# Kernel tuning notes

Measured on AMD Instinct MI355X. Metric: run time of the kernel, lower is better.

## Reference

```python
import jax, jax.numpy as jnp
import numpy as np

NUM_BITS = 8
NUM_STEPS = 2 ** NUM_BITS - 2  # 254, clamp range -127..127


def _roundpass(x):
    # straight-through round: forward=round, backward=identity
    return x + jax.lax.stop_gradient(jnp.round(x) - x)


def _quantize(x, alpha, always_pos=False):
    # Quantizer.quantize with use_ste=True, is_on=True
    alpha = jax.nn.relu(alpha)  # relu(alpha_baseline + alpha_delta)
    stepsize = 2.0 * alpha / NUM_STEPS
    off = alpha if always_pos else 0.0
    scaled = (x - off) / stepsize
    clamped = jnp.clip(_roundpass(scaled), -(NUM_STEPS // 2), NUM_STEPS // 2)
    return clamped * stepsize + off


def setup_inputs() -> dict:
    key = jax.random.key(0)
    k1, k2 = jax.random.split(key)
    x = jax.random.normal(k1, (32, 64, 56, 56), dtype=jnp.float32)
    w = jax.random.normal(k2, (128, 64, 3, 3), dtype=jnp.float32) * 0.05
    alpha_x = jnp.ones((1,), dtype=jnp.float32)
    alpha_w = jnp.ones((1,), dtype=jnp.float32)
    return {"x": x, "w": w, "alpha_x": alpha_x, "alpha_w": alpha_w}


def reference(x, w, alpha_x, alpha_w):
    # quantize activations and weights (8-bit symmetric, STE round)
    qx = _quantize(x, alpha_x[0], always_pos=False)
    qw = _quantize(w, alpha_w[0], always_pos=False)
    # im2col lowering + tiled_mm accumulation over K-tiles is exactly a
    # stride-1 conv with padding (1,1); tile padding in M/N/K contributes
    # only zeros and is sliced off, so plain conv is the faithful math.
    out = jax.lax.conv_general_dilated(
        qx, qw,
        window_strides=(1, 1),
        padding=((1, 1), (1, 1)),
        dimension_numbers=("NCHW", "OIHW", "NCHW"),
    )  # [32, 128, 56, 56]
    return out
```

## Files before the change

kernel.cpp:

```cpp
#include <hip/hip_runtime.h>
#include <hip/hip_bf16.h>

typedef int   v4i __attribute__((ext_vector_type(4)));
typedef float v4f __attribute__((ext_vector_type(4)));

#define HWSZ 3136
#define IMW  56
#define PADW 58
#define PHW  3364
#define CIN  64
#define COUT 128

__device__ __forceinline__ float step_size(float a) {
    a = a > 0.f ? a : 0.f;
    return 2.0f * a / 254.0f;
}

__device__ __forceinline__ int quant1(float x, float s) {
    float v = rintf(x / s);
    v = fminf(127.f, fmaxf(-127.f, v));
    return (int)v;
}

__device__ __forceinline__ unsigned int pack4(int a, int b, int c, int d) {
    return (unsigned int)(a & 255) | ((unsigned int)(b & 255) << 8) |
           ((unsigned int)(c & 255) << 16) | ((unsigned int)(d & 255) << 24);
}

__device__ __forceinline__ void gload_lds16(const signed char* g, signed char* l) {
    __builtin_amdgcn_global_load_lds(
        (const __attribute__((address_space(1))) void*)g,
        (__attribute__((address_space(3))) void*)l, 16, 0, 0);
}

__global__ __launch_bounds__(256) void quant_kernel(const float* __restrict__ x,
                                                    const float* __restrict__ w,
                                                    const float* __restrict__ alpha_x,
                                                    const float* __restrict__ alpha_w,
                                                    signed char* __restrict__ cx,
                                                    signed char* __restrict__ wt) {
    int t = threadIdx.x;
    int b = blockIdx.x;
    if (b >= 1568) {
        if (b >= 1856) {
            int q = (b - 1856) * 256 + t;
            int n = q / 912;
            int r = q % 912;
            int px = r >> 2, seg = r & 3;
            int ph, pw;
            if (px < 58)       { ph = 0;  pw = px; }
            else if (px < 116) { ph = 57; pw = px - 58; }
            else { int k = px - 116; ph = 1 + (k >> 1); pw = (k & 1) * 57; }
            v4i z = {0, 0, 0, 0};
            *(v4i*)(cx + ((size_t)n * PHW + ph * PADW + pw) * 64 + seg * 16) = z;
            return;
        }
        float s = step_size(alpha_w[0]);
        int j = (b - 1568) * 256 + t;
        int tap = j / 8192;
        int r   = j % 8192;
        int o   = r >> 6;
        int c   = r & 63;
        float v = w[((size_t)o * 64 + c) * 9 + tap];
        wt[j] = (signed char)quant1(v, s);
        return;
    }

    __shared__ unsigned int tile32[64 * 17];
    float s = step_size(alpha_x[0]);
    int n   = b / 49;
    int hw0 = (b % 49) * 64;
    int g   = t & 15;
    int cq  = t >> 4;
    int p   = t >> 2;
    int seg = t & 3;

    const float* xb = x + ((size_t)n * CIN + cq * 4) * HWSZ + hw0 + g * 4;
    v4f f0 = *(const v4f*)(xb);
    v4f f1 = *(const v4f*)(xb + HWSZ);
    v4f f2 = *(const v4f*)(xb + 2 * HWSZ);
    v4f f3 = *(const v4f*)(xb + 3 * HWSZ);
#pragma unroll
    for (int j = 0; j < 4; ++j) {
        unsigned int u = pack4(quant1(f0[j], s), quant1(f1[j], s),
                               quant1(f2[j], s), quant1(f3[j], s));
        tile32[(g * 4 + j) * 17 + cq] = u;
    }
    __syncthreads();
    int base = p * 17 + seg * 4;
    v4i val;
    val[0] = (int)tile32[base + 0];
    val[1] = (int)tile32[base + 1];
    val[2] = (int)tile32[base + 2];
    val[3] = (int)tile32[base + 3];
    int hw = hw0 + p;
    int h = hw / IMW, wq = hw % IMW;
    *(v4i*)(cx + ((size_t)n * PHW + (h + 1) * PADW + (wq + 1)) * 64 + seg * 16) = val;
}

__global__ __launch_bounds__(256, 4) void conv_kernel(const signed char* __restrict__ cx,
                                                      const signed char* __restrict__ wt,
                                                      const float* __restrict__ ax,
                                                      const float* __restrict__ aw,
                                                      float* __restrict__ out) {
    __shared__ __attribute__((aligned(16))) signed char as_[34816];
    float scale = step_size(ax[0]) * step_size(aw[0]);
    int tid  = threadIdx.x;
    int lane = tid & 63;
    int wid  = tid >> 6;
    int row  = lane & 15;
    int kg   = lane >> 4;

    int bid  = blockIdx.x;
    int swz  = (bid & 7) * 196 + (bid >> 3);
    int p0   = swz * 64;
    int n    = p0 / HWSZ;
    int hw0  = p0 % HWSZ;
    int h0   = hw0 / IMW;
    int us   = h0 - 1; if (us > 52) us = 52;

    const signed char* wsrc = cx + ((size_t)n * PHW + (size_t)(us + 1) * PADW) * 64;
#pragma unroll
    for (int r = 0; r < 5; ++r) {
        int slotbase = r * 256 + wid * 64;
        gload_lds16(wsrc + (size_t)(slotbase + lane) * 16, as_ + slotbase * 16);
    }

    int obase = wid * 32;
    const signed char* wb = wt + (obase + row) * 64 + kg * 16;
    v4i breg[9][2];
#pragma unroll
    for (int tap = 0; tap < 9; ++tap)
#pragma unroll
        for (int ot = 0; ot < 2; ++ot)
            breg[tap][ot] = *(const v4i*)(wb + tap * (COUT * 64) + ot * (16 * 64));

    int lbase[4];
#pragma unroll
    for (int pt = 0; pt < 4; ++pt) {
        int hwp = hw0 + pt * 16 + row;
        int hh  = hwp / IMW, ww = hwp % IMW;
        lbase[pt] = ((hh - us) * PADW + (ww + 1)) * 64 + kg * 16;
    }

    asm volatile("s_waitcnt vmcnt(0)" ::: "memory");
    __syncthreads();
#pragma unroll
    for (int tap = 0; tap < 9; ++tap)
#pragma unroll
        for (int ot = 0; ot < 2; ++ot)
            asm volatile("" :: "v"(breg[tap][ot]));

    v4i acc[4][2] = {};
#pragma unroll
    for (int tap = 0; tap < 9; ++tap) {
        int doff = ((tap / 3 - 1) * PADW + (tap % 3 - 1)) * 64;
        v4i a[4];
#pragma unroll
        for (int pt = 0; pt < 4; ++pt)
            a[pt] = *(const v4i*)(as_ + lbase[pt] + doff);
#pragma unroll
        for (int pt = 0; pt < 4; ++pt)
#pragma unroll
            for (int ot = 0; ot < 2; ++ot)
                acc[pt][ot] = __builtin_amdgcn_mfma_i32_16x16x64_i8(a[pt], breg[tap][ot], acc[pt][ot], 0, 0, 0);
    }

    __syncthreads();
    signed char* scrw = as_ + wid * 8704;
    float* obb = out + ((size_t)n * COUT) * HWSZ + hw0;

#pragma unroll
    for (int otl = 0; otl < 2; ++otl) {
        int ol = otl * 16 + row;
#pragma unroll
        for (int pt = 0; pt < 4; ++pt) {
            int c  = pt * 4 + kg;
            int cs = c ^ (ol & 7);
            v4f v;
            v[0] = scale * (float)acc[pt][otl][0];
            v[1] = scale * (float)acc[pt][otl][1];
            v[2] = scale * (float)acc[pt][otl][2];
            v[3] = scale * (float)acc[pt][otl][3];
            *(v4f*)(scrw + ol * 272 + cs * 16) = v;
        }
    }
    {
        int og = lane >> 4;
        int c  = lane & 15;
#pragma unroll
        for (int j = 0; j < 8; ++j) {
            int ol = j * 4 + og;
            int cs = c ^ (ol & 7);
            v4f v = *(const v4f*)(scrw + ol * 272 + cs * 16);
            int o = obase + ol;
            *(v4f*)(obb + (size_t)o * HWSZ + c * 4) = v;
        }
    }
}

extern "C" void kernel_launch(void* const* d_in, const int* in_sizes, int n_in,
                              void* d_out, int out_size, void* d_ws, size_t ws_size,
                              hipStream_t stream) {
    const float* x  = (const float*)d_in[0];
    const float* w  = (const float*)d_in[1];
    const float* ax = (const float*)d_in[2];
    const float* aw = (const float*)d_in[3];
    float* out = (float*)d_out;

    signed char* cx = (signed char*)d_ws;
    signed char* wt = cx + 6889472;

    quant_kernel<<<1970, 256, 0, stream>>>(x, w, ax, aw, cx, wt);
    conv_kernel<<<1568, 256, 0, stream>>>(cx, wt, ax, aw, out);
}
```

Baseline: 29.15 us.

## Fuse activation quantization into conv kernel, drop padded int8 intermediate

Activation quantization and padding move into the conv kernel. Each block loads its five input rows of fp32 straight from x, quantizes them to int8, and writes them transposed into LDS, with zeroed halo rows and columns. This removes the global write and re-read of the padded int8 activation tensor and the extra launch work for it, leaving only a small weight-quantization kernel. In exchange each input row is read and quantized by several overlapping blocks (5 rows loaded per 64-pixel tile, about 4x redundancy in fp32 reads), and the LDS stores are scattered 4-byte writes.

Result: slower. 39.58 us (+35.8%).

```diff
diff --git a/kernel.cpp b/kernel.cpp
--- a/kernel.cpp
+++ b/kernel.cpp
@@ -6,10 +6,9 @@
 
 #define HWSZ 3136
 #define IMW  56
-#define PADW 58
-#define PHW  3364
 #define CIN  64
 #define COUT 128
+#define ROWB 3712
 
 __device__ __forceinline__ float step_size(float a) {
     a = a > 0.f ? a : 0.f;
@@ -27,84 +26,26 @@
            ((unsigned int)(c & 255) << 16) | ((unsigned int)(d & 255) << 24);
 }
 
-__device__ __forceinline__ void gload_lds16(const signed char* g, signed char* l) {
-    __builtin_amdgcn_global_load_lds(
-        (const __attribute__((address_space(1))) void*)g,
-        (__attribute__((address_space(3))) void*)l, 16, 0, 0);
+__global__ __launch_bounds__(256) void quantw_kernel(const float* __restrict__ w,
+                                                     const float* __restrict__ alpha_w,
+                                                     signed char* __restrict__ wt) {
+    float s = step_size(alpha_w[0]);
+    int j = blockIdx.x * 256 + threadIdx.x;
+    int tap = j / 8192;
+    int r   = j % 8192;
+    int o   = r >> 6;
+    int c   = r & 63;
+    wt[j] = (signed char)quant1(w[((size_t)o * 64 + c) * 9 + tap], s);
 }
 
-__global__ __launch_bounds__(256) void quant_kernel(const float* __restrict__ x,
-                                                    const float* __restrict__ w,
-                                                    const float* __restrict__ alpha_x,
-                                                    const float* __restrict__ alpha_w,
-                                                    signed char* __restrict__ cx,
-                                                    signed char* __restrict__ wt) {
-    int t = threadIdx.x;
-    int b = blockIdx.x;
-    if (b >= 1568) {
-        if (b >= 1856) {
-            int q = (b - 1856) * 256 + t;
-            int n = q / 912;
-            int r = q % 912;
-            int px = r >> 2, seg = r & 3;
-            int ph, pw;
-            if (px < 58)       { ph = 0;  pw = px; }
-            else if (px < 116) { ph = 57; pw = px - 58; }
-            else { int k = px - 116; ph = 1 + (k >> 1); pw = (k & 1) * 57; }
-            v4i z = {0, 0, 0, 0};
-            *(v4i*)(cx + ((size_t)n * PHW + ph * PADW + pw) * 64 + seg * 16) = z;
-            return;
-        }
-        float s = step_size(alpha_w[0]);
-        int j = (b - 1568) * 256 + t;
-        int tap = j / 8192;
-        int r   = j % 8192;
-        int o   = r >> 6;
-        int c   = r & 63;
-        float v = w[((size_t)o * 64 + c) * 9 + tap];
-        wt[j] = (signed char)quant1(v, s);
-        return;
-    }
-
-    __shared__ unsigned int tile32[64 * 17];
-    float s = step_size(alpha_x[0]);
-    int n   = b / 49;
-    int hw0 = (b % 49) * 64;
-    int g   = t & 15;
-    int cq  = t >> 4;
-    int p   = t >> 2;
-    int seg = t & 3;
-
-    const float* xb = x + ((size_t)n * CIN + cq * 4) * HWSZ + hw0 + g * 4;
-    v4f f0 = *(const v4f*)(xb);
-    v4f f1 = *(const v4f*)(xb + HWSZ);
-    v4f f2 = *(const v4f*)(xb + 2 * HWSZ);
-    v4f f3 = *(const v4f*)(xb + 3 * HWSZ);
-#pragma unroll
-    for (int j = 0; j < 4; ++j) {
-        unsigned int u = pack4(quant1(f0[j], s), quant1(f1[j], s),
-                               quant1(f2[j], s), quant1(f3[j], s));
-        tile32[(g * 4 + j) * 17 + cq] = u;
-    }
-    __syncthreads();
-    int base = p * 17 + seg * 4;
-    v4i val;
-    val[0] = (int)tile32[base + 0];
-    val[1] = (int)tile32[base + 1];
-    val[2] = (int)tile32[base + 2];
-    val[3] = (int)tile32[base + 3];
-    int hw = hw0 + p;
-    int h = hw / IMW, wq = hw % IMW;
-    *(v4i*)(cx + ((size_t)n * PHW + (h + 1) * PADW + (wq + 1)) * 64 + seg * 16) = val;
-}
-
-__global__ __launch_bounds__(256, 4) void conv_kernel(const signed char* __restrict__ cx,
+__global__ __launch_bounds__(256, 4) void conv_kernel(const float* __restrict__ x,
                                                       const signed char* __restrict__ wt,
                                                       const float* __restrict__ ax,
                                                       const float* __restrict__ aw,
                                                       float* __restrict__ out) {
     __shared__ __attribute__((aligned(16))) signed char as_[34816];
-    float scale = step_size(ax[0]) * step_size(aw[0]);
+    float sx    = step_size(ax[0]);
+    float scale = sx * step_size(aw[0]);
     int tid  = threadIdx.x;
     int lane = tid & 63;
     int wid  = tid >> 6;
@@ -119,13 +60,6 @@
     int h0   = hw0 / IMW;
     int us   = h0 - 1; if (us > 52) us = 52;
 
-    const signed char* wsrc = cx + ((size_t)n * PHW + (size_t)(us + 1) * PADW) * 64;
-#pragma unroll
-    for (int r = 0; r < 5; ++r) {
-        int slotbase = r * 256 + wid * 64;
-        gload_lds16(wsrc + (size_t)(slotbase + lane) * 16, as_ + slotbase * 16);
-    }
-
     int obase = wid * 32;
     const signed char* wb = wt + (obase + row) * 64 + kg * 16;
     v4i breg[9][2];
@@ -135,15 +69,49 @@
         for (int ot = 0; ot < 2; ++ot)
             breg[tap][ot] = *(const v4i*)(wb + tap * (COUT * 64) + ot * (16 * 64));
 
+    {
+        int g  = tid & 15;
+        int cq = tid >> 4;
+#pragma unroll
+        for (int r = 0; r < 5; ++r) {
+            int u = us + r;
+            signed char* lrow = as_ + r * ROWB;
+            if (u < 0 || u > 55) {
+                unsigned int* lp = (unsigned int*)lrow;
+#pragma unroll
+                for (int k = 0; k < 4; ++k) {
+                    int idx = k * 256 + tid;
+                    if (idx < 928) lp[idx] = 0;
+                }
+            } else {
+                if (g < 14) {
+                    const float* xb = x + (size_t)(n * CIN + cq * 4) * HWSZ + u * IMW + g * 4;
+                    v4f f0 = *(const v4f*)(xb);
+                    v4f f1 = *(const v4f*)(xb + HWSZ);
+                    v4f f2 = *(const v4f*)(xb + 2 * HWSZ);
+                    v4f f3 = *(const v4f*)(xb + 3 * HWSZ);
+#pragma unroll
+                    for (int j = 0; j < 4; ++j) {
+                        unsigned int uq = pack4(quant1(f0[j], sx), quant1(f1[j], sx),
+                                                quant1(f2[j], sx), quant1(f3[j], sx));
+                        *(unsigned int*)(lrow + (1 + g * 4 + j) * 64 + cq * 4) = uq;
+                    }
+                } else if (g == 14) {
+                    *(unsigned int*)(lrow + cq * 4) = 0;
+                    *(unsigned int*)(lrow + 57 * 64 + cq * 4) = 0;
+                }
+            }
+        }
+    }
+
     int lbase[4];
 #pragma unroll
     for (int pt = 0; pt < 4; ++pt) {
         int hwp = hw0 + pt * 16 + row;
         int hh  = hwp / IMW, ww = hwp % IMW;
-        lbase[pt] = ((hh - us) * PADW + (ww + 1)) * 64 + kg * 16;
+        lbase[pt] = (hh - us) * ROWB + (ww + 1) * 64 + kg * 16;
     }
 
-    asm volatile("s_waitcnt vmcnt(0)" ::: "memory");
     __syncthreads();
 #pragma unroll
     for (int tap = 0; tap < 9; ++tap)
@@ -154,7 +122,7 @@
     v4i acc[4][2] = {};
 #pragma unroll
     for (int tap = 0; tap < 9; ++tap) {
-        int doff = ((tap / 3 - 1) * PADW + (tap % 3 - 1)) * 64;
+        int doff = (tap / 3 - 1) * ROWB + (tap % 3 - 1) * 64;
         v4i a[4];
 #pragma unroll
         for (int pt = 0; pt < 4; ++pt)
@@ -208,9 +176,8 @@
     const float* aw = (const float*)d_in[3];
     float* out = (float*)d_out;
 
-    signed char* cx = (signed char*)d_ws;
-    signed char* wt = cx + 6889472;
+    signed char* wt = (signed char*)d_ws;
 
-    quant_kernel<<<1970, 256, 0, stream>>>(x, w, ax, aw, cx, wt);
-    conv_kernel<<<1568, 256, 0, stream>>>(cx, wt, ax, aw, out);
+    quantw_kernel<<<288, 256, 0, stream>>>(w, aw, wt);
+    conv_kernel<<<1568, 256, 0, stream>>>(x, wt, ax, aw, out);
 }
```

## Enlarge conv tile to two image rows per block, cutting halo reloads

Applied to the files above, without the earlier changes.

Each conv block now covers 112 pixels (two full image rows) instead of 64, loading 4 padded rows into LDS rather than 5. That reduces redundant halo traffic, lets each wave reuse its register-held weights across 7 pixel tiles, and lowers the block count from 1568 to 896. The epilogue is reorganised into two passes through a smaller LDS scratch buffer. In exchange, register pressure grows (occupancy hint drops from 4 to 3), and the store phase leaves some lanes idle and adds an explicit wait.

New measurement: 34.39 us. +18.0%, slower.

```diff
diff --git a/kernel.cpp b/kernel.cpp
--- a/kernel.cpp
+++ b/kernel.cpp
@@ -10,6 +10,7 @@
 #define PHW  3364
 #define CIN  64
 #define COUT 128
+#define ROWB 3712
 
 __device__ __forceinline__ float step_size(float a) {
     a = a > 0.f ? a : 0.f;
@@ -98,12 +99,12 @@
     *(v4i*)(cx + ((size_t)n * PHW + (h + 1) * PADW + (wq + 1)) * 64 + seg * 16) = val;
 }
 
-__global__ __launch_bounds__(256, 4) void conv_kernel(const signed char* __restrict__ cx,
+__global__ __launch_bounds__(256, 3) void conv_kernel(const signed char* __restrict__ cx,
                                                       const signed char* __restrict__ wt,
                                                       const float* __restrict__ ax,
                                                       const float* __restrict__ aw,
                                                       float* __restrict__ out) {
-    __shared__ __attribute__((aligned(16))) signed char as_[34816];
+    __shared__ __attribute__((aligned(16))) signed char as_[29184];
     float scale = step_size(ax[0]) * step_size(aw[0]);
     int tid  = threadIdx.x;
     int lane = tid & 63;
@@ -111,17 +112,17 @@
     int row  = lane & 15;
     int kg   = lane >> 4;
 
-    int bid  = blockIdx.x;
-    int swz  = (bid & 7) * 196 + (bid >> 3);
-    int p0   = swz * 64;
-    int n    = p0 / HWSZ;
-    int hw0  = p0 % HWSZ;
-    int h0   = hw0 / IMW;
-    int us   = h0 - 1; if (us > 52) us = 52;
-
-    const signed char* wsrc = cx + ((size_t)n * PHW + (size_t)(us + 1) * PADW) * 64;
-#pragma unroll
-    for (int r = 0; r < 5; ++r) {
+    int bid = blockIdx.x;
+    int swz = (bid & 7) * 112 + (bid >> 3);
+    int n   = swz / 28;
+    int tl  = swz % 28;
+    int hw0 = tl * 112;
+    int h0  = tl * 2;
+    int us  = h0 - 1;
+
+    const signed char* wsrc = cx + ((size_t)n * PHW + (size_t)h0 * PADW) * 64;
+#pragma unroll
+    for (int r = 0; r < 4; ++r) {
         int slotbase = r * 256 + wid * 64;
         gload_lds16(wsrc + (size_t)(slotbase + lane) * 16, as_ + slotbase * 16);
     }
@@ -135,12 +136,12 @@
         for (int ot = 0; ot < 2; ++ot)
             breg[tap][ot] = *(const v4i*)(wb + tap * (COUT * 64) + ot * (16 * 64));
 
-    int lbase[4];
-#pragma unroll
-    for (int pt = 0; pt < 4; ++pt) {
+    int lbase[7];
+#pragma unroll
+    for (int pt = 0; pt < 7; ++pt) {
         int hwp = hw0 + pt * 16 + row;
         int hh  = hwp / IMW, ww = hwp % IMW;
-        lbase[pt] = ((hh - us) * PADW + (ww + 1)) * 64 + kg * 16;
+        lbase[pt] = (hh - us) * ROWB + (ww + 1) * 64 + kg * 16;
     }
 
     asm volatile("s_waitcnt vmcnt(0)" ::: "memory");
@@ -151,51 +152,50 @@
         for (int ot = 0; ot < 2; ++ot)
             asm volatile("" :: "v"(breg[tap][ot]));
 
-    v4i acc[4][2] = {};
+    v4i acc[7][2] = {};
 #pragma unroll
     for (int tap = 0; tap < 9; ++tap) {
-        int doff = ((tap / 3 - 1) * PADW + (tap % 3 - 1)) * 64;
-        v4i a[4];
-#pragma unroll
-        for (int pt = 0; pt < 4; ++pt)
+        int doff = (tap / 3 - 1) * ROWB + (tap % 3 - 1) * 64;
+        v4i a[7];
+#pragma unroll
+        for (int pt = 0; pt < 7; ++pt)
             a[pt] = *(const v4i*)(as_ + lbase[pt] + doff);
 #pragma unroll
-        for (int pt = 0; pt < 4; ++pt)
+        for (int pt = 0; pt < 7; ++pt)
 #pragma unroll
             for (int ot = 0; ot < 2; ++ot)
                 acc[pt][ot] = __builtin_amdgcn_mfma_i32_16x16x64_i8(a[pt], breg[tap][ot], acc[pt][ot], 0, 0, 0);
     }
 
     __syncthreads();
-    signed char* scrw = as_ + wid * 8704;
+    signed char* scrw = as_ + wid * 7296;
     float* obb = out + ((size_t)n * COUT) * HWSZ + hw0;
-
-#pragma unroll
-    for (int otl = 0; otl < 2; ++otl) {
-        int ol = otl * 16 + row;
-#pragma unroll
-        for (int pt = 0; pt < 4; ++pt) {
-            int c  = pt * 4 + kg;
-            int cs = c ^ (ol & 7);
+    int og = lane >> 5;
+    (void)og;
+
+#pragma unroll
+    for (int rr = 0; rr < 2; ++rr) {
+#pragma unroll
+        for (int pt = 0; pt < 7; ++pt) {
             v4f v;
-            v[0] = scale * (float)acc[pt][otl][0];
-            v[1] = scale * (float)acc[pt][otl][1];
-            v[2] = scale * (float)acc[pt][otl][2];
-            v[3] = scale * (float)acc[pt][otl][3];
-            *(v4f*)(scrw + ol * 272 + cs * 16) = v;
+            v[0] = scale * (float)acc[pt][rr][0];
+            v[1] = scale * (float)acc[pt][rr][1];
+            v[2] = scale * (float)acc[pt][rr][2];
+            v[3] = scale * (float)acc[pt][rr][3];
+            *(v4f*)(scrw + row * 456 + pt * 64 + kg * 16) = v;
         }
-    }
-    {
-        int og = lane >> 4;
-        int c  = lane & 15;
-#pragma unroll
-        for (int j = 0; j < 8; ++j) {
-            int ol = j * 4 + og;
-            int cs = c ^ (ol & 7);
-            v4f v = *(const v4f*)(scrw + ol * 272 + cs * 16);
-            int o = obase + ol;
-            *(v4f*)(obb + (size_t)o * HWSZ + c * 4) = v;
+        if (lane < 56) {
+            int g2 = lane / 28;
+            int c  = lane - g2 * 28;
+#pragma unroll
+            for (int j = 0; j < 8; ++j) {
+                int ol = j * 2 + g2;
+                v4f v = *(const v4f*)(scrw + ol * 456 + c * 16);
+                int o = obase + rr * 16 + ol;
+                *(v4f*)(obb + (size_t)o * HWSZ + c * 4) = v;
+            }
         }
+        __builtin_amdgcn_s_waitcnt(0);
     }
 }
 
@@ -212,5 +212,5 @@
     signed char* wt = cx + 6889472;
 
     quant_kernel<<<1970, 256, 0, stream>>>(x, w, ax, aw, cx, wt);
-    conv_kernel<<<1568, 256, 0, stream>>>(cx, wt, ax, aw, out);
-}
+    conv_kernel<<<896, 256, 0, stream>>>(cx, wt, ax, aw, out);
+}
```
